# Kernel tuning notes

Measured on AMD Instinct MI355X. Metric: run time of the kernel, lower is better.

Reference implementation:

```python
import jax, jax.numpy as jnp
import numpy as np
from math import sqrt

KERNEL = 25
INV_SQRT2 = 1.0 / sqrt(2.0)


def _moving_avg(xt):
    # xt: [B, L]; replicate-pad then average-pool k=25 stride=1 -> [B, L]
    pad_l = (KERNEL - 1) // 2
    pad_r = KERNEL - 1 - pad_l
    xp = jnp.pad(xt, ((0, 0), (pad_l, pad_r)), mode='edge')[:, None, :]  # [B,1,Lp]
    k = jnp.full((1, 1, KERNEL), 1.0 / KERNEL, dtype=xt.dtype)  # [O,I,W]
    out = jax.lax.conv_general_dilated(xp, k, window_strides=(1,), padding='VALID',
                                       dimension_numbers=('NCH', 'OIH', 'NCH'))
    return out[:, 0, :]


def setup_inputs() -> dict:
    key = jax.random.key(0)
    ks = jax.random.split(key, 7)
    B, L, P, H = 8192, 4096, 720, 2048
    return {
        'x': jax.random.normal(ks[0], (B, L, 1), dtype=jnp.float32),
        'W_trend': jax.random.normal(ks[1], (P, L), dtype=jnp.float32) * 0.02,
        'b_trend': jax.random.normal(ks[2], (P,), dtype=jnp.float32) * 0.02,
        'W_lo': jax.random.normal(ks[3], (P, H), dtype=jnp.float32) * 0.02,
        'b_lo': jax.random.normal(ks[4], (P,), dtype=jnp.float32) * 0.02,
        'W_hi': jax.random.normal(ks[5], (P, H), dtype=jnp.float32) * 0.02,
        'b_hi': jax.random.normal(ks[6], (P,), dtype=jnp.float32) * 0.02,
    }


def reference(x, W_trend, b_trend, W_lo, b_lo, W_hi, b_hi):
    xt = x[..., 0]                              # [B, L]
    trend = _moving_avg(xt)                     # [B, L]
    res = xt - trend                            # [B, L]
    res_mean = jnp.mean(res, axis=-1, keepdims=True)
    # torch.std is unbiased (ddof=1)
    res_std = jnp.std(res, axis=-1, keepdims=True, ddof=1) + 1e-5
    res_norm = (res - res_mean) / res_std       # [B, L]
    # Haar DWT (stride-2 conv with [1,1]/sqrt2 and [1,-1]/sqrt2); L even -> no pad
    even, odd = res_norm[:, 0::2], res_norm[:, 1::2]  # [B, L/2]
    res_lo = (even + odd) * INV_SQRT2
    res_hi = (even - odd) * INV_SQRT2
    pred_trend = trend @ W_trend.T + b_trend    # [B, P]
    pred_res = (res_lo @ W_lo.T + b_lo) + (res_hi @ W_hi.T + b_hi)
    total = pred_trend + pred_res * res_std     # res_std broadcasts [B,1]
    return total[..., None]                     # [B, P, 1]
```

## Files before the change

### kernel.cpp

```cpp
#include <hip/hip_runtime.h>

typedef unsigned short u16;
typedef unsigned int   u32;
typedef __attribute__((ext_vector_type(8))) short bf16x8;
typedef __attribute__((ext_vector_type(4))) float f32x4;

#define LROW 4096
#define NB   8192
#define PCOL 720
#define NPAD 768
#define HH   2048
#define INV_SQRT2F 0.70710678118654752440f

#define WS_XBF_BYTES ((size_t)67108864)
#define WS_G_BYTES   ((size_t)6291456)
#define WS_MIN       (WS_XBF_BYTES + WS_G_BYTES + (size_t)NB * 4)

__device__ __forceinline__ u16 f2bf(float f) {
    union { float f; u32 u; } v; v.f = f;
    u32 r = v.u + 0x7FFFu + ((v.u >> 16) & 1u);
    return (u16)(r >> 16);
}

#define SWZ(i) ((i) ^ (((i) >> 5) & 31))

__global__ __launch_bounds__(256) void prep_rows(const float* __restrict__ x,
                                                 u16* __restrict__ xbf,
                                                 float* __restrict__ stdv) {
    __shared__ float S[LROW];
    __shared__ float wred[4];
    __shared__ float ends[2];
    __shared__ float rred[8];
    const int tid = threadIdx.x;
    const int lane = tid & 63, wv = tid >> 6;
    const size_t b = blockIdx.x;

    const float4* xr4 = (const float4*)(x + b * LROW);
    float4 q0 = xr4[tid * 4 + 0], q1 = xr4[tid * 4 + 1];
    float4 q2 = xr4[tid * 4 + 2], q3 = xr4[tid * 4 + 3];
    float r[16];
    r[0]=q0.x; r[1]=q0.y; r[2]=q0.z; r[3]=q0.w;
    r[4]=q1.x; r[5]=q1.y; r[6]=q1.z; r[7]=q1.w;
    r[8]=q2.x; r[9]=q2.y; r[10]=q2.z; r[11]=q2.w;
    r[12]=q3.x; r[13]=q3.y; r[14]=q3.z; r[15]=q3.w;

    float ps[16];
    float a = 0.f;
    #pragma unroll
    for (int k = 0; k < 16; ++k) { a += r[k]; ps[k] = a; }
    const float segsum = a;

    float v = segsum;
    #pragma unroll
    for (int off = 1; off < 64; off <<= 1) {
        float o = __shfl_up(v, off);
        if (lane >= off) v += o;
    }
    if (lane == 63) wred[wv] = v;
    if (tid == 0)   ends[0] = r[0];
    if (tid == 255) ends[1] = r[15];
    __syncthreads();

    float wbase = 0.f;
    #pragma unroll
    for (int w = 0; w < 4; ++w) if (w < wv) wbase += wred[w];
    const float ebase = wbase + v - segsum;

    #pragma unroll
    for (int k = 0; k < 16; ++k) {
        const int i = (tid << 4) + k;
        S[SWZ(i)] = ebase + ps[k];
    }
    __syncthreads();

    const float x0 = ends[0], xl = ends[1];
    float s1 = 0.f, s2 = 0.f;
    u16 ob[16];
    #pragma unroll
    for (int k = 0; k < 16; ++k) {
        const int i = (tid << 4) + k;
        int h = i + 12; h = h > LROW - 1 ? LROW - 1 : h;
        float wsum = S[SWZ(h)];
        if (i >= 13) wsum -= S[SWZ(i - 13)];
        if (i < 12) wsum += (float)(12 - i) * x0;
        if (i > LROW - 13) wsum += (float)(i - (LROW - 13)) * xl;
        const float xi = r[k];
        const float rr = xi - wsum * 0.04f;
        s1 += rr; s2 += rr * rr;
        ob[k] = f2bf(xi);
    }

    uint4 o0, o1;
    o0.x = (u32)ob[0]  | ((u32)ob[1]  << 16);
    o0.y = (u32)ob[2]  | ((u32)ob[3]  << 16);
    o0.z = (u32)ob[4]  | ((u32)ob[5]  << 16);
    o0.w = (u32)ob[6]  | ((u32)ob[7]  << 16);
    o1.x = (u32)ob[8]  | ((u32)ob[9]  << 16);
    o1.y = (u32)ob[10] | ((u32)ob[11] << 16);
    o1.z = (u32)ob[12] | ((u32)ob[13] << 16);
    o1.w = (u32)ob[14] | ((u32)ob[15] << 16);
    uint4* op = (uint4*)(xbf + b * LROW + ((size_t)tid << 4));
    op[0] = o0; op[1] = o1;

    #pragma unroll
    for (int off = 32; off; off >>= 1) {
        s1 += __shfl_down(s1, off);
        s2 += __shfl_down(s2, off);
    }
    if (lane == 0) { rred[wv * 2] = s1; rred[wv * 2 + 1] = s2; }
    __syncthreads();
    if (tid == 0) {
        const float S1 = rred[0] + rred[2] + rred[4] + rred[6];
        const float S2 = rred[1] + rred[3] + rred[5] + rred[7];
        const float mean = S1 / (float)LROW;
        float var = (S2 - (float)LROW * mean * mean) / (float)(LROW - 1);
        var = var < 0.f ? 0.f : var;
        stdv[b] = sqrtf(var) + 1e-5f;
    }
}

__global__ __launch_bounds__(256) void prep_weights(const float* __restrict__ Wt,
                                                    const float* __restrict__ Wlo,
                                                    const float* __restrict__ Whi,
                                                    u16* __restrict__ Gm) {
    __shared__ float S[LROW];
    __shared__ float wred[4];
    __shared__ float sred[4];
    const int tid = threadIdx.x;
    const int lane = tid & 63, wv = tid >> 6;
    const int p = blockIdx.x;
    u16* grow = Gm + (size_t)p * LROW;
    if (p >= PCOL) {
        uint4 z; z.x = z.y = z.z = z.w = 0u;
        uint4* g4 = (uint4*)grow;
        for (int i = tid; i < LROW / 8; i += 256) g4[i] = z;
        return;
    }
    const float4* wt4 = (const float4*)(Wt + (size_t)p * LROW);
    float4 q0 = wt4[tid * 4 + 0], q1 = wt4[tid * 4 + 1];
    float4 q2 = wt4[tid * 4 + 2], q3 = wt4[tid * 4 + 3];
    const float4* lo4 = (const float4*)(Wlo + (size_t)p * HH);
    const float4* hi4 = (const float4*)(Whi + (size_t)p * HH);
    float4 a0 = lo4[tid * 2 + 0], a1 = lo4[tid * 2 + 1];
    float4 b0 = hi4[tid * 2 + 0], b1 = hi4[tid * 2 + 1];

    float w[16];
    w[0]=q0.x; w[1]=q0.y; w[2]=q0.z; w[3]=q0.w;
    w[4]=q1.x; w[5]=q1.y; w[6]=q1.z; w[7]=q1.w;
    w[8]=q2.x; w[9]=q2.y; w[10]=q2.z; w[11]=q2.w;
    w[12]=q3.x; w[13]=q3.y; w[14]=q3.z; w[15]=q3.w;
    float lv[8] = {a0.x,a0.y,a0.z,a0.w,a1.x,a1.y,a1.z,a1.w};
    float hv[8] = {b0.x,b0.y,b0.z,b0.w,b1.x,b1.y,b1.z,b1.w};

    float u[16], z_[16];
    float slo = 0.f;
    #pragma unroll
    for (int j = 0; j < 8; ++j) {
        u[2*j]   = (lv[j] + hv[j]) * INV_SQRT2F;
        u[2*j+1] = (lv[j] - hv[j]) * INV_SQRT2F;
        slo += lv[j];
    }
    #pragma unroll
    for (int k = 0; k < 16; ++k) z_[k] = w[k] - u[k];

    float ps[16];
    float a = 0.f;
    #pragma unroll
    for (int k = 0; k < 16; ++k) { a += z_[k]; ps[k] = a; }
    const float segsum = a;

    float v = segsum;
    #pragma unroll
    for (int off = 1; off < 64; off <<= 1) {
        float o = __shfl_up(v, off);
        if (lane >= off) v += o;
    }
    if (lane == 63) wred[wv] = v;
    #pragma unroll
    for (int off = 32; off; off >>= 1) slo += __shfl_down(slo, off);
    if (lane == 0) sred[wv] = slo;
    __syncthreads();

    float wbase = 0.f;
    #pragma unroll
    for (int ww = 0; ww < 4; ++ww) if (ww < wv) wbase += wred[ww];
    const float ebase = wbase + v - segsum;
    const float SLO = sred[0] + sred[1] + sred[2] + sred[3];

    #pragma unroll
    for (int k = 0; k < 16; ++k) {
        const int i = (tid << 4) + k;
        S[SWZ(i)] = ebase + ps[k];
    }
    __syncthreads();

    const float coef = -1.4142135623730951f * SLO / (float)LROW;
    u16 ob[16];
    #pragma unroll
    for (int k = 0; k < 16; ++k) {
        const int l = (tid << 4) + k;
        float zT;
        if (l == 0) {
            float acc = 0.f;
            for (int m = 0; m <= 12; ++m) acc += S[SWZ(m)];
            zT = acc * 0.04f;
        } else if (l == LROW - 1) {
            float acc = 0.f;
            for (int m = 0; m <= 12; ++m) acc += S[SWZ(LROW - 2 - m)];
            zT = (13.f * S[SWZ(LROW - 1)] - acc) * 0.04f;
        } else {
            int h = l + 12; h = h > LROW - 1 ? LROW - 1 : h;
            float t_ = S[SWZ(h)];
            if (l >= 13) t_ -= S[SWZ(l - 13)];
            zT = t_ * 0.04f;
        }
        float c;
        const int dmin = l < (LROW - 1 - l) ? l : (LROW - 1 - l);
        if (dmin >= 12)      c = 0.f;
        else if (dmin == 0)  c = -66.f / 25.f;
        else                 c = (float)(12 - dmin) * 0.04f;
        ob[k] = f2bf(zT + u[k] + coef * c);
    }

    uint4 o0, o1;
    o0.x = (u32)ob[0]  | ((u32)ob[1]  << 16);
    o0.y = (u32)ob[2]  | ((u32)ob[3]  << 16);
    o0.z = (u32)ob[4]  | ((u32)ob[5]  << 16);
    o0.w = (u32)ob[6]  | ((u32)ob[7]  << 16);
    o1.x = (u32)ob[8]  | ((u32)ob[9]  << 16);
    o1.y = (u32)ob[10] | ((u32)ob[11] << 16);
    o1.z = (u32)ob[12] | ((u32)ob[13] << 16);
    o1.w = (u32)ob[14] | ((u32)ob[15] << 16);
    uint4* op = (uint4*)(grow + ((size_t)tid << 4));
    op[0] = o0; op[1] = o1;
}

typedef __attribute__((address_space(1))) void gvoid;
typedef __attribute__((address_space(3))) void lvoid;
#define GLD16(g, l_) __builtin_amdgcn_global_load_lds((gvoid*)(g), (lvoid*)(l_), 16, 0, 0)
#define MF(a, b, c) __builtin_amdgcn_mfma_f32_16x16x32_bf16(a, b, c, 0, 0, 0)

#define ABUFB 16384
#define BBASE 49152
#define BBUFB 12288

#define STAGE_B(T, DB) do { \
    char* d_ = Sm + BBASE + (DB) * BBUFB + wid * 3072; \
    const size_t go_ = (size_t)(T) * 128; \
    GLD16(sB0 + go_, d_); \
    GLD16(sB0 + go_ + 65536, d_ + 1024); \
    GLD16(sB0 + go_ + 131072, d_ + 2048); \
} while (0)

#define STAGE_A(T, DB) do { \
    char* d_ = Sm + (DB) * ABUFB + wid * 4096; \
    const size_t go_ = (size_t)(T) * 128; \
    GLD16(sA0 + go_, d_); \
    GLD16(sA0 + go_ + 65536, d_ + 1024); \
    GLD16(sA0 + go_ + 131072, d_ + 2048); \
    GLD16(sA0 + go_ + 196608, d_ + 3072); \
} while (0)

#define ITER(T, AB, BB, SBB, SAB, VM, SB, SA) do { \
    asm volatile("s_waitcnt vmcnt(" #VM ")" ::: "memory"); \
    __builtin_amdgcn_s_barrier(); \
    __builtin_amdgcn_sched_barrier(0); \
    if (SB) STAGE_B((T) + 1, SBB); \
    if (SA) STAGE_A((T) + 2, SAB); \
    __builtin_amdgcn_sched_barrier(0); \
    const char* a_ = Sm + (AB) * ABUFB + aro; \
    const char* b_ = Sm + BBASE + (BB) * BBUFB + bro; \
    bf16x8 A0 = *(const bf16x8*)(a_); \
    bf16x8 A1 = *(const bf16x8*)(a_ + 2048); \
    bf16x8 A2 = *(const bf16x8*)(a_ + 4096); \
    bf16x8 A3 = *(const bf16x8*)(a_ + 6144); \
    bf16x8 B0 = *(const bf16x8*)(b_); \
    bf16x8 B1 = *(const bf16x8*)(b_ + 2048); \
    bf16x8 B2 = *(const bf16x8*)(b_ + 4096); \
    bf16x8 B3 = *(const bf16x8*)(b_ + 6144); \
    bf16x8 B4 = *(const bf16x8*)(b_ + 8192); \
    bf16x8 B5 = *(const bf16x8*)(b_ + 10240); \
    asm volatile("s_waitcnt lgkmcnt(0)" ::: "memory"); \
    __builtin_amdgcn_sched_barrier(0); \
    __builtin_amdgcn_s_setprio(1); \
    acc[0][0]=MF(A0,B0,acc[0][0]); acc[0][1]=MF(A0,B1,acc[0][1]); acc[0][2]=MF(A0,B2,acc[0][2]); \
    acc[0][3]=MF(A0,B3,acc[0][3]); acc[0][4]=MF(A0,B4,acc[0][4]); acc[0][5]=MF(A0,B5,acc[0][5]); \
    acc[1][0]=MF(A1,B0,acc[1][0]); acc[1][1]=MF(A1,B1,acc[1][1]); acc[1][2]=MF(A1,B2,acc[1][2]); \
    acc[1][3]=MF(A1,B3,acc[1][3]); acc[1][4]=MF(A1,B4,acc[1][4]); acc[1][5]=MF(A1,B5,acc[1][5]); \
    acc[2][0]=MF(A2,B0,acc[2][0]); acc[2][1]=MF(A2,B1,acc[2][1]); acc[2][2]=MF(A2,B2,acc[2][2]); \
    acc[2][3]=MF(A2,B3,acc[2][3]); acc[2][4]=MF(A2,B4,acc[2][4]); acc[2][5]=MF(A2,B5,acc[2][5]); \
    acc[3][0]=MF(A3,B0,acc[3][0]); acc[3][1]=MF(A3,B1,acc[3][1]); acc[3][2]=MF(A3,B2,acc[3][2]); \
    acc[3][3]=MF(A3,B3,acc[3][3]); acc[3][4]=MF(A3,B4,acc[3][4]); acc[3][5]=MF(A3,B5,acc[3][5]); \
    __builtin_amdgcn_s_setprio(0); \
} while (0)

__global__ __launch_bounds__(256, 2) void gemm_fused(const u16* __restrict__ Abf,
                                                     const u16* __restrict__ Gbf,
                                                     const float* __restrict__ bt,
                                                     const float* __restrict__ bl,
                                                     const float* __restrict__ bh,
                                                     const float* __restrict__ stdv,
                                                     float* __restrict__ out) {
    __shared__ __align__(16) char Sm[73728];
    const int tid = threadIdx.x;
    const int l = tid & 63, wid = tid >> 6;
    const int wm = wid & 1, kp = wid >> 1;

    const int orig = blockIdx.x;
    const int chunk = orig & 7, pos = orig >> 3;
    const int bx = pos & 7;
    const int by = (chunk << 3) + (pos >> 3);
    const int m0 = by * 128;
    const int n0 = bx * 96;

    const int sgb = (((l & 7) ^ (l >> 3)) << 4);
    const char* sA0 = (const char*)Abf + ((size_t)(m0 + wid * 32 + (l >> 3)) << 13) + sgb;
    const char* sB0 = (const char*)Gbf + ((size_t)(n0 + wid * 24 + (l >> 3)) << 13) + sgb;

    const int slot16 = ((((kp << 2) + (l >> 4)) ^ (l & 7)) << 4);
    const int aro = (wm * 64 + (l & 15)) * 128 + slot16;
    const int bro = (l & 15) * 128 + slot16;

    f32x4 acc[4][6] = {};

    STAGE_A(0, 0);
    STAGE_A(1, 1);
    STAGE_B(0, 0);

    ITER(        0, 0, 0, 1,  2, 0, 1, 1);
    for (int t = 1; t <= 55; t += 6) {
        ITER(t    , 1, 1, 0, 0, 4, 1, 1);
        ITER(t + 1, 2, 0, 1, 1, 4, 1, 1);
        ITER(t + 2, 0, 1, 0, 2, 4, 1, 1);
        ITER(t + 3, 1, 0, 1, 0, 4, 1, 1);
        ITER(t + 4, 2, 1, 0, 1, 4, 1, 1);
        ITER(t + 5, 0, 0, 1, 2, 4, 1, 1);
    }
    ITER(61, 1, 1, 0, 0, 4, 1, 1);
    ITER(62, 2, 0, 1, 0, 4, 1, 0);
    ITER(63, 0, 1, 0, 0, 0, 0, 0);

    __syncthreads();
    float* red = (float*)Sm;
    const int rr = (l >> 4) << 2;
    const int cc = l & 15;
    const int rbase = wm * 6528;
    if (kp == 1) {
        #pragma unroll
        for (int m = 0; m < 4; ++m)
            #pragma unroll
            for (int n = 0; n < 6; ++n)
                *(f32x4*)(red + rbase + (n * 16 + cc) * 68 + m * 16 + rr) = acc[m][n];
    }
    __syncthreads();
    if (kp == 0) {
        const int crow = m0 + wm * 64 + rr;
        const int ccol = n0 + cc;
        float btv[6], bsv[6];
        #pragma unroll
        for (int n = 0; n < 6; ++n) {
            const int col = ccol + n * 16;
            if (col < PCOL) { btv[n] = bt[col]; bsv[n] = bl[col] + bh[col]; }
            else            { btv[n] = 0.f; bsv[n] = 0.f; }
        }
        #pragma unroll
        for (int m = 0; m < 4; ++m) {
            const int row = crow + m * 16;
            const float4 sv = *(const float4*)(stdv + row);
            #pragma unroll
            for (int n = 0; n < 6; ++n) {
                const int col = ccol + n * 16;
                if (col < PCOL) {
                    const f32x4 pv = *(const f32x4*)(red + rbase + (n * 16 + cc) * 68 + m * 16 + rr);
                    float* orow = out + (size_t)row * PCOL + col;
                    #pragma unroll
                    for (int j = 0; j < 4; ++j) {
                        const float s = (j == 0) ? sv.x : (j == 1) ? sv.y : (j == 2) ? sv.z : sv.w;
                        orow[(size_t)j * PCOL] = acc[m][n][j] + pv[j] + btv[n] + s * bsv[n];
                    }
                }
            }
        }
    }
}

extern "C" void kernel_launch(void* const* d_in, const int* in_sizes, int n_in,
                              void* d_out, int out_size, void* d_ws, size_t ws_size,
                              hipStream_t stream) {
    (void)in_sizes; (void)n_in; (void)out_size;
    if (ws_size < WS_MIN) return;

    const float* x  = (const float*)d_in[0];
    const float* Wt = (const float*)d_in[1];
    const float* bt = (const float*)d_in[2];
    const float* Wl = (const float*)d_in[3];
    const float* bl = (const float*)d_in[4];
    const float* Wh = (const float*)d_in[5];
    const float* bh = (const float*)d_in[6];
    float* out = (float*)d_out;

    char* ws = (char*)d_ws;
    u16*   xbf = (u16*)ws;
    u16*   Gm  = (u16*)(ws + WS_XBF_BYTES);
    float* sd  = (float*)(ws + WS_XBF_BYTES + WS_G_BYTES);

    prep_rows<<<NB, 256, 0, stream>>>(x, xbf, sd);
    prep_weights<<<NPAD, 256, 0, stream>>>(Wt, Wl, Wh, Gm);
    gemm_fused<<<512, 256, 0, stream>>>(xbf, Gm, bt, bl, bh, sd, out);
}
```

Before: 97.29 us.

## Double-buffer MFMA fragments in registers and merge A/B LDS staging

The GEMM main loop changes from a three-buffer A / two-buffer B LDS ring to a unified two-stage A+B ring. LDS fragments for the next k-tile are read into a second register set while the MFMAs for the current tile run, so LDS read latency overlaps with compute. Shared memory drops from 72KB to 56KB. In exchange, each iteration now waits with vmcnt(0), which shortens global-load prefetch depth to about one iteration, and the extra fragment registers raise VGPR pressure.

```diff
diff --git a/kernel.cpp b/kernel.cpp
--- a/kernel.cpp
+++ b/kernel.cpp
@@ -241,56 +241,57 @@
 #define MF(a, b, c) __builtin_amdgcn_mfma_f32_16x16x32_bf16(a, b, c, 0, 0, 0)
 
 #define ABUFB 16384
-#define BBASE 49152
+#define BBASE 32768
 #define BBUFB 12288
 
-#define STAGE_B(T, DB) do { \
-    char* d_ = Sm + BBASE + (DB) * BBUFB + wid * 3072; \
+#define STAGE_AB(T, DB) do { \
+    char* da_ = Sm + (DB) * ABUFB + wid * 4096; \
+    char* db_ = Sm + BBASE + (DB) * BBUFB + wid * 3072; \
     const size_t go_ = (size_t)(T) * 128; \
-    GLD16(sB0 + go_, d_); \
-    GLD16(sB0 + go_ + 65536, d_ + 1024); \
-    GLD16(sB0 + go_ + 131072, d_ + 2048); \
+    GLD16(sA0 + go_, da_); \
+    GLD16(sA0 + go_ + 65536, da_ + 1024); \
+    GLD16(sA0 + go_ + 131072, da_ + 2048); \
+    GLD16(sA0 + go_ + 196608, da_ + 3072); \
+    GLD16(sB0 + go_, db_); \
+    GLD16(sB0 + go_ + 65536, db_ + 1024); \
+    GLD16(sB0 + go_ + 131072, db_ + 2048); \
 } while (0)
 
-#define STAGE_A(T, DB) do { \
-    char* d_ = Sm + (DB) * ABUFB + wid * 4096; \
-    const size_t go_ = (size_t)(T) * 128; \
-    GLD16(sA0 + go_, d_); \
-    GLD16(sA0 + go_ + 65536, d_ + 1024); \
-    GLD16(sA0 + go_ + 131072, d_ + 2048); \
-    GLD16(sA0 + go_ + 196608, d_ + 3072); \
+#define READ_FRAGS(P, BUF) do { \
+    const char* a_ = Sm + (BUF) * ABUFB + aro; \
+    const char* b_ = Sm + BBASE + (BUF) * BBUFB + bro; \
+    P##A0 = *(const bf16x8*)(a_); \
+    P##A1 = *(const bf16x8*)(a_ + 2048); \
+    P##A2 = *(const bf16x8*)(a_ + 4096); \
+    P##A3 = *(const bf16x8*)(a_ + 6144); \
+    P##B0 = *(const bf16x8*)(b_); \
+    P##B1 = *(const bf16x8*)(b_ + 2048); \
+    P##B2 = *(const bf16x8*)(b_ + 4096); \
+    P##B3 = *(const bf16x8*)(b_ + 6144); \
+    P##B4 = *(const bf16x8*)(b_ + 8192); \
+    P##B5 = *(const bf16x8*)(b_ + 10240); \
 } while (0)
 
-#define ITER(T, AB, BB, SBB, SAB, VM, SB, SA) do { \
-    asm volatile("s_waitcnt vmcnt(" #VM ")" ::: "memory"); \
+#define MFMA24(P) do { \
+    acc[0][0]=MF(P##A0,P##B0,acc[0][0]); acc[0][1]=MF(P##A0,P##B1,acc[0][1]); acc[0][2]=MF(P##A0,P##B2,acc[0][2]); \
+    acc[0][3]=MF(P##A0,P##B3,acc[0][3]); acc[0][4]=MF(P##A0,P##B4,acc[0][4]); acc[0][5]=MF(P##A0,P##B5,acc[0][5]); \
+    acc[1][0]=MF(P##A1,P##B0,acc[1][0]); acc[1][1]=MF(P##A1,P##B1,acc[1][1]); acc[1][2]=MF(P##A1,P##B2,acc[1][2]); \
+    acc[1][3]=MF(P##A1,P##B3,acc[1][3]); acc[1][4]=MF(P##A1,P##B4,acc[1][4]); acc[1][5]=MF(P##A1,P##B5,acc[1][5]); \
+    acc[2][0]=MF(P##A2,P##B0,acc[2][0]); acc[2][1]=MF(P##A2,P##B1,acc[2][1]); acc[2][2]=MF(P##A2,P##B2,acc[2][2]); \
+    acc[2][3]=MF(P##A2,P##B3,acc[2][3]); acc[2][4]=MF(P##A2,P##B4,acc[2][4]); acc[2][5]=MF(P##A2,P##B5,acc[2][5]); \
+    acc[3][0]=MF(P##A3,P##B0,acc[3][0]); acc[3][1]=MF(P##A3,P##B1,acc[3][1]); acc[3][2]=MF(P##A3,P##B2,acc[3][2]); \
+    acc[3][3]=MF(P##A3,P##B3,acc[3][3]); acc[3][4]=MF(P##A3,P##B4,acc[3][4]); acc[3][5]=MF(P##A3,P##B5,acc[3][5]); \
+} while (0)
+
+#define ITER(T, CUR, NXT, DOSTAGE, DOREAD) do { \
+    asm volatile("s_waitcnt vmcnt(0) lgkmcnt(0)" ::: "memory"); \
     __builtin_amdgcn_s_barrier(); \
     __builtin_amdgcn_sched_barrier(0); \
-    if (SB) STAGE_B((T) + 1, SBB); \
-    if (SA) STAGE_A((T) + 2, SAB); \
-    __builtin_amdgcn_sched_barrier(0); \
-    const char* a_ = Sm + (AB) * ABUFB + aro; \
-    const char* b_ = Sm + BBASE + (BB) * BBUFB + bro; \
-    bf16x8 A0 = *(const bf16x8*)(a_); \
-    bf16x8 A1 = *(const bf16x8*)(a_ + 2048); \
-    bf16x8 A2 = *(const bf16x8*)(a_ + 4096); \
-    bf16x8 A3 = *(const bf16x8*)(a_ + 6144); \
-    bf16x8 B0 = *(const bf16x8*)(b_); \
-    bf16x8 B1 = *(const bf16x8*)(b_ + 2048); \
-    bf16x8 B2 = *(const bf16x8*)(b_ + 4096); \
-    bf16x8 B3 = *(const bf16x8*)(b_ + 6144); \
-    bf16x8 B4 = *(const bf16x8*)(b_ + 8192); \
-    bf16x8 B5 = *(const bf16x8*)(b_ + 10240); \
-    asm volatile("s_waitcnt lgkmcnt(0)" ::: "memory"); \
+    if (DOSTAGE) STAGE_AB((T) + 2, (T) & 1); \
+    if (DOREAD) READ_FRAGS(NXT, ((T) + 1) & 1); \
     __builtin_amdgcn_sched_barrier(0); \
     __builtin_amdgcn_s_setprio(1); \
-    acc[0][0]=MF(A0,B0,acc[0][0]); acc[0][1]=MF(A0,B1,acc[0][1]); acc[0][2]=MF(A0,B2,acc[0][2]); \
-    acc[0][3]=MF(A0,B3,acc[0][3]); acc[0][4]=MF(A0,B4,acc[0][4]); acc[0][5]=MF(A0,B5,acc[0][5]); \
-    acc[1][0]=MF(A1,B0,acc[1][0]); acc[1][1]=MF(A1,B1,acc[1][1]); acc[1][2]=MF(A1,B2,acc[1][2]); \
-    acc[1][3]=MF(A1,B3,acc[1][3]); acc[1][4]=MF(A1,B4,acc[1][4]); acc[1][5]=MF(A1,B5,acc[1][5]); \
-    acc[2][0]=MF(A2,B0,acc[2][0]); acc[2][1]=MF(A2,B1,acc[2][1]); acc[2][2]=MF(A2,B2,acc[2][2]); \
-    acc[2][3]=MF(A2,B3,acc[2][3]); acc[2][4]=MF(A2,B4,acc[2][4]); acc[2][5]=MF(A2,B5,acc[2][5]); \
-    acc[3][0]=MF(A3,B0,acc[3][0]); acc[3][1]=MF(A3,B1,acc[3][1]); acc[3][2]=MF(A3,B2,acc[3][2]); \
-    acc[3][3]=MF(A3,B3,acc[3][3]); acc[3][4]=MF(A3,B4,acc[3][4]); acc[3][5]=MF(A3,B5,acc[3][5]); \
+    MFMA24(CUR); \
     __builtin_amdgcn_s_setprio(0); \
 } while (0)
 
@@ -301,7 +302,7 @@
                                                      const float* __restrict__ bh,
                                                      const float* __restrict__ stdv,
                                                      float* __restrict__ out) {
-    __shared__ __align__(16) char Sm[73728];
+    __shared__ __align__(16) char Sm[57344];
     const int tid = threadIdx.x;
     const int l = tid & 63, wid = tid >> 6;
     const int wm = wid & 1, kp = wid >> 1;
@@ -322,23 +323,24 @@
     const int bro = (l & 15) * 128 + slot16;
 
     f32x4 acc[4][6] = {};
-
-    STAGE_A(0, 0);
-    STAGE_A(1, 1);
-    STAGE_B(0, 0);
-
-    ITER(        0, 0, 0, 1,  2, 0, 1, 1);
-    for (int t = 1; t <= 55; t += 6) {
-        ITER(t    , 1, 1, 0, 0, 4, 1, 1);
-        ITER(t + 1, 2, 0, 1, 1, 4, 1, 1);
-        ITER(t + 2, 0, 1, 0, 2, 4, 1, 1);
-        ITER(t + 3, 1, 0, 1, 0, 4, 1, 1);
-        ITER(t + 4, 2, 1, 0, 1, 4, 1, 1);
-        ITER(t + 5, 0, 0, 1, 2, 4, 1, 1);
-    }
-    ITER(61, 1, 1, 0, 0, 4, 1, 1);
-    ITER(62, 2, 0, 1, 0, 4, 1, 0);
-    ITER(63, 0, 1, 0, 0, 0, 0, 0);
+    bf16x8 XA0, XA1, XA2, XA3, XB0, XB1, XB2, XB3, XB4, XB5;
+    bf16x8 YA0, YA1, YA2, YA3, YB0, YB1, YB2, YB3, YB4, YB5;
+
+    STAGE_AB(0, 0);
+    STAGE_AB(1, 1);
+    asm volatile("s_waitcnt vmcnt(7)" ::: "memory");
+    __builtin_amdgcn_s_barrier();
+    __builtin_amdgcn_sched_barrier(0);
+    READ_FRAGS(X, 0);
+
+    for (int t = 0; t < 60; t += 2) {
+        ITER(t,     X, Y, 1, 1);
+        ITER(t + 1, Y, X, 1, 1);
+    }
+    ITER(60, X, Y, 1, 1);
+    ITER(61, Y, X, 1, 1);
+    ITER(62, X, Y, 0, 1);
+    ITER(63, Y, X, 0, 0);
 
     __syncthreads();
     float* red = (float*)Sm;
```

Result: no change. 95.39 us (-1.9%).

## Prefetch next A fragment into registers during MFMAs and change LDS layout

Applied to the files above, without the earlier changes.

Restructures the GEMM main loop so the A-operand LDS reads for the next k-step are issued right after the current MFMA block, into alternating X/Y register sets, instead of at the start of each iteration. The global-to-LDS staging layout also changes from XOR-swizzled 128-byte rows to per-wave quadrant tiles with 64-byte row stride, with matching read offsets. The aim is to hide LDS read latency behind matrix math and reduce the lgkmcnt wait before MFMAs. It costs extra registers for the double-buffered A fragments. Dropping the swizzle may introduce LDS bank conflicts, and the finer vmcnt bookkeeping must be exactly right.

```diff
diff --git a/kernel.cpp b/kernel.cpp
--- a/kernel.cpp
+++ b/kernel.cpp
@@ -244,54 +244,75 @@
 #define BBASE 49152
 #define BBUFB 12288
 
+#define STAGE_A(T, DB) do { \
+    char* d_ = Sm + (DB) * ABUFB + aqb; \
+    const size_t go_ = (size_t)(T) * 128; \
+    GLD16(sA + go_,          d_); \
+    GLD16(sA + go_ + 131072, d_ + 1024); \
+    GLD16(sA + go_ + 262144, d_ + 2048); \
+    GLD16(sA + go_ + 393216, d_ + 3072); \
+} while (0)
+
 #define STAGE_B(T, DB) do { \
-    char* d_ = Sm + BBASE + (DB) * BBUFB + wid * 3072; \
+    char* d_ = Sm + BBASE + (DB) * BBUFB + bqb; \
     const size_t go_ = (size_t)(T) * 128; \
-    GLD16(sB0 + go_, d_); \
-    GLD16(sB0 + go_ + 65536, d_ + 1024); \
-    GLD16(sB0 + go_ + 131072, d_ + 2048); \
-} while (0)
-
-#define STAGE_A(T, DB) do { \
-    char* d_ = Sm + (DB) * ABUFB + wid * 4096; \
-    const size_t go_ = (size_t)(T) * 128; \
-    GLD16(sA0 + go_, d_); \
-    GLD16(sA0 + go_ + 65536, d_ + 1024); \
-    GLD16(sA0 + go_ + 131072, d_ + 2048); \
-    GLD16(sA0 + go_ + 196608, d_ + 3072); \
-} while (0)
-
-#define ITER(T, AB, BB, SBB, SAB, VM, SB, SA) do { \
-    asm volatile("s_waitcnt vmcnt(" #VM ")" ::: "memory"); \
+    GLD16(sB + go_,          d_); \
+    GLD16(sB + go_ + 131072, d_ + 1024); \
+    GLD16(sB + go_ + 262144, d_ + 2048); \
+} while (0)
+
+#define READ_B(DB) do { \
+    const char* b_ = Sm + BBASE + (DB) * BBUFB + bro; \
+    B0 = *(const bf16x8*)(b_); \
+    B1 = *(const bf16x8*)(b_ + 1024); \
+    B2 = *(const bf16x8*)(b_ + 2048); \
+    B3 = *(const bf16x8*)(b_ + 3072); \
+    B4 = *(const bf16x8*)(b_ + 4096); \
+    B5 = *(const bf16x8*)(b_ + 5120); \
+} while (0)
+
+#define READ_A(P, DB) do { \
+    const char* a_ = Sm + (DB) * ABUFB + aro; \
+    P##0 = *(const bf16x8*)(a_); \
+    P##1 = *(const bf16x8*)(a_ + 1024); \
+    P##2 = *(const bf16x8*)(a_ + 2048); \
+    P##3 = *(const bf16x8*)(a_ + 3072); \
+} while (0)
+
+#define MFMA24(P) do { \
+    acc[0][0]=MF(P##0,B0,acc[0][0]); acc[1][0]=MF(P##1,B0,acc[1][0]); \
+    acc[2][0]=MF(P##2,B0,acc[2][0]); acc[3][0]=MF(P##3,B0,acc[3][0]); \
+    acc[0][1]=MF(P##0,B1,acc[0][1]); acc[1][1]=MF(P##1,B1,acc[1][1]); \
+    acc[2][1]=MF(P##2,B1,acc[2][1]); acc[3][1]=MF(P##3,B1,acc[3][1]); \
+    acc[0][2]=MF(P##0,B2,acc[0][2]); acc[1][2]=MF(P##1,B2,acc[1][2]); \
+    acc[2][2]=MF(P##2,B2,acc[2][2]); acc[3][2]=MF(P##3,B2,acc[3][2]); \
+    acc[0][3]=MF(P##0,B3,acc[0][3]); acc[1][3]=MF(P##1,B3,acc[1][3]); \
+    acc[2][3]=MF(P##2,B3,acc[2][3]); acc[3][3]=MF(P##3,B3,acc[3][3]); \
+    acc[0][4]=MF(P##0,B4,acc[0][4]); acc[1][4]=MF(P##1,B4,acc[1][4]); \
+    acc[2][4]=MF(P##2,B4,acc[2][4]); acc[3][4]=MF(P##3,B4,acc[3][4]); \
+    acc[0][5]=MF(P##0,B5,acc[0][5]); acc[1][5]=MF(P##1,B5,acc[1][5]); \
+    acc[2][5]=MF(P##2,B5,acc[2][5]); acc[3][5]=MF(P##3,B5,acc[3][5]); \
+} while (0)
+
+#define ITER(T, CUR, NXT, ARD, AST, BRD, BST, V1, V2, SB, SA, RDA) do { \
+    asm volatile("s_waitcnt vmcnt(" #V1 ")" ::: "memory"); \
     __builtin_amdgcn_s_barrier(); \
     __builtin_amdgcn_sched_barrier(0); \
-    if (SB) STAGE_B((T) + 1, SBB); \
-    if (SA) STAGE_A((T) + 2, SAB); \
+    if (SB) STAGE_B((T) + 1, BST); \
+    if (SA) STAGE_A((T) + 2, AST); \
     __builtin_amdgcn_sched_barrier(0); \
-    const char* a_ = Sm + (AB) * ABUFB + aro; \
-    const char* b_ = Sm + BBASE + (BB) * BBUFB + bro; \
-    bf16x8 A0 = *(const bf16x8*)(a_); \
-    bf16x8 A1 = *(const bf16x8*)(a_ + 2048); \
-    bf16x8 A2 = *(const bf16x8*)(a_ + 4096); \
-    bf16x8 A3 = *(const bf16x8*)(a_ + 6144); \
-    bf16x8 B0 = *(const bf16x8*)(b_); \
-    bf16x8 B1 = *(const bf16x8*)(b_ + 2048); \
-    bf16x8 B2 = *(const bf16x8*)(b_ + 4096); \
-    bf16x8 B3 = *(const bf16x8*)(b_ + 6144); \
-    bf16x8 B4 = *(const bf16x8*)(b_ + 8192); \
-    bf16x8 B5 = *(const bf16x8*)(b_ + 10240); \
+    READ_B(BRD); \
     asm volatile("s_waitcnt lgkmcnt(0)" ::: "memory"); \
     __builtin_amdgcn_sched_barrier(0); \
     __builtin_amdgcn_s_setprio(1); \
-    acc[0][0]=MF(A0,B0,acc[0][0]); acc[0][1]=MF(A0,B1,acc[0][1]); acc[0][2]=MF(A0,B2,acc[0][2]); \
-    acc[0][3]=MF(A0,B3,acc[0][3]); acc[0][4]=MF(A0,B4,acc[0][4]); acc[0][5]=MF(A0,B5,acc[0][5]); \
-    acc[1][0]=MF(A1,B0,acc[1][0]); acc[1][1]=MF(A1,B1,acc[1][1]); acc[1][2]=MF(A1,B2,acc[1][2]); \
-    acc[1][3]=MF(A1,B3,acc[1][3]); acc[1][4]=MF(A1,B4,acc[1][4]); acc[1][5]=MF(A1,B5,acc[1][5]); \
-    acc[2][0]=MF(A2,B0,acc[2][0]); acc[2][1]=MF(A2,B1,acc[2][1]); acc[2][2]=MF(A2,B2,acc[2][2]); \
-    acc[2][3]=MF(A2,B3,acc[2][3]); acc[2][4]=MF(A2,B4,acc[2][4]); acc[2][5]=MF(A2,B5,acc[2][5]); \
-    acc[3][0]=MF(A3,B0,acc[3][0]); acc[3][1]=MF(A3,B1,acc[3][1]); acc[3][2]=MF(A3,B2,acc[3][2]); \
-    acc[3][3]=MF(A3,B3,acc[3][3]); acc[3][4]=MF(A3,B4,acc[3][4]); acc[3][5]=MF(A3,B5,acc[3][5]); \
+    MFMA24(CUR); \
     __builtin_amdgcn_s_setprio(0); \
+    __builtin_amdgcn_sched_barrier(0); \
+    if (RDA) { \
+        asm volatile("s_waitcnt vmcnt(" #V2 ")" ::: "memory"); \
+        __builtin_amdgcn_sched_barrier(0); \
+        READ_A(NXT, ARD); \
+    } \
 } while (0)
 
 __global__ __launch_bounds__(256, 2) void gemm_fused(const u16* __restrict__ Abf,
@@ -313,32 +334,40 @@
     const int m0 = by * 128;
     const int n0 = bx * 96;
 
-    const int sgb = (((l & 7) ^ (l >> 3)) << 4);
-    const char* sA0 = (const char*)Abf + ((size_t)(m0 + wid * 32 + (l >> 3)) << 13) + sgb;
-    const char* sB0 = (const char*)Gbf + ((size_t)(n0 + wid * 24 + (l >> 3)) << 13) + sgb;
-
-    const int slot16 = ((((kp << 2) + (l >> 4)) ^ (l & 7)) << 4);
-    const int aro = (wm * 64 + (l & 15)) * 128 + slot16;
-    const int bro = (l & 15) * 128 + slot16;
+    const char* sA = (const char*)Abf
+        + ((size_t)(m0 + wm * 64 + (l >> 2)) << 13) + kp * 64 + ((l & 3) << 4);
+    const char* sB = (const char*)Gbf
+        + ((size_t)(n0 + wm * 48 + (l >> 2)) << 13) + kp * 64 + ((l & 3) << 4);
+    const int aqb = wm * 8192 + kp * 4096;
+    const int bqb = kp * 6144 + wm * 3072;
+
+    const int aro = wm * 8192 + kp * 4096 + ((l & 15) << 6) + ((l >> 4) << 4);
+    const int bro = kp * 6144 + ((l & 15) << 6) + ((l >> 4) << 4);
 
     f32x4 acc[4][6] = {};
+    bf16x8 X0, X1, X2, X3, Y0, Y1, Y2, Y3;
+    bf16x8 B0, B1, B2, B3, B4, B5;
 
     STAGE_A(0, 0);
+    STAGE_B(0, 0);
     STAGE_A(1, 1);
-    STAGE_B(0, 0);
-
-    ITER(        0, 0, 0, 1,  2, 0, 1, 1);
-    for (int t = 1; t <= 55; t += 6) {
-        ITER(t    , 1, 1, 0, 0, 4, 1, 1);
-        ITER(t + 1, 2, 0, 1, 1, 4, 1, 1);
-        ITER(t + 2, 0, 1, 0, 2, 4, 1, 1);
-        ITER(t + 3, 1, 0, 1, 0, 4, 1, 1);
-        ITER(t + 4, 2, 1, 0, 1, 4, 1, 1);
-        ITER(t + 5, 0, 0, 1, 2, 4, 1, 1);
-    }
-    ITER(61, 1, 1, 0, 0, 4, 1, 1);
-    ITER(62, 2, 0, 1, 0, 4, 1, 0);
-    ITER(63, 0, 1, 0, 0, 0, 0, 0);
+    asm volatile("s_waitcnt vmcnt(4)" ::: "memory");
+    __builtin_amdgcn_s_barrier();
+    __builtin_amdgcn_sched_barrier(0);
+    READ_A(X, 0);
+
+    for (int t = 0; t < 60; t += 6) {
+        ITER(t + 0, X, Y, 1, 2, 0, 1, 4, 7, 1, 1, 1);
+        ITER(t + 1, Y, X, 2, 0, 1, 0, 4, 7, 1, 1, 1);
+        ITER(t + 2, X, Y, 0, 1, 0, 1, 4, 7, 1, 1, 1);
+        ITER(t + 3, Y, X, 1, 2, 1, 0, 4, 7, 1, 1, 1);
+        ITER(t + 4, X, Y, 2, 0, 0, 1, 4, 7, 1, 1, 1);
+        ITER(t + 5, Y, X, 0, 1, 1, 0, 4, 7, 1, 1, 1);
+    }
+    ITER(60, X, Y, 1, 2, 0, 1, 4, 7, 1, 1, 1);
+    ITER(61, Y, X, 2, 0, 1, 0, 4, 7, 1, 1, 1);
+    ITER(62, X, Y, 0, 0, 0, 1, 4, 3, 1, 0, 1);
+    ITER(63, Y, X, 0, 0, 1, 0, 0, 0, 0, 0, 0);
 
     __syncthreads();
     float* red = (float*)Sm;
```

Result: no change. 98.23 us (+1.0%).
